# Optimization experiments

Hardware: AMD Instinct MI355X
Metric: run time of the kernel (lower is better)

The kernel has to match this reference:

```python
import jax, jax.numpy as jnp
import numpy as np

D = 64       # latent channels (d)
T = 512      # frame length, pinned by fc_1 = Linear(512*d//2, 512)
NUM_M = 64   # codebook size for source half (num_s = num_m)
NUM_N = 32   # codebook size for noise half (num_n = num_m // 2)
SCALE = 1.0  # soft-assignment temperature (self.scale)
K = 9        # BasicBlock conv kernel width


def conv1d(x, w, b):
    # x: (B, Cin, T), w: (Cout, Cin, K) -> (B, Cout, T), SAME padding
    y = jax.lax.conv_general_dilated(
        x, w, window_strides=(1,), padding='SAME',
        dimension_numbers=('NCH', 'OIH', 'NCH'))
    return y + b[None, :, None]


def basic_block(x, w1, b1, w2, b2, ws=None, bs=None):
    # Residual 1-D conv block: conv-relu-conv + shortcut, relu.
    h = jax.nn.relu(conv1d(x, w1, b1))
    h = conv1d(h, w2, b2)
    sc = x if ws is None else conv1d(x, ws, bs)
    return jax.nn.relu(h + sc)


def code_assign(x, means, scale):
    # VQ-style soft codebook assignment.
    # x: (B, C, T), means: (C, M)
    xt = jnp.swapaxes(x, 1, 2)  # (B, T, C)
    d2 = (jnp.sum(xt * xt, axis=-1, keepdims=True)
          - 2.0 * jnp.einsum('btc,cm->btm', xt, means)
          + jnp.sum(means * means, axis=0)[None, None, :])  # (B, T, M) squared dists
    prob = jax.nn.softmax(-scale * d2, axis=-1)              # soft assignment
    q = jnp.einsum('btm,cm->bct', prob, means)               # (B, C, T)
    arg_idx = jnp.argmin(d2, axis=-1)                        # (B, T) hard code index
    return q, arg_idx


def setup_inputs() -> dict:
    key = jax.random.key(0)
    ks = jax.random.split(key, 10)
    s = 0.05
    B = 1024
    return {
        'x': jax.random.normal(ks[0], (B, T), jnp.float32),
        'enc0_w1': jax.random.normal(ks[1], (D, 1, K), jnp.float32) * s,
        'enc0_b1': jnp.zeros((D,), jnp.float32),
        'enc0_w2': jax.random.normal(ks[2], (D, D, K), jnp.float32) * s,
        'enc0_b2': jnp.zeros((D,), jnp.float32),
        'enc0_ws': jax.random.normal(ks[3], (D, 1, 1), jnp.float32) * s,
        'enc0_bs': jnp.zeros((D,), jnp.float32),
        'enc_w': jax.random.normal(ks[4], (3, 2, D, D, K), jnp.float32) * s,
        'enc_b': jnp.zeros((3, 2, D), jnp.float32),
        'dec_w': jax.random.normal(ks[5], (3, 2, D // 2, D // 2, K), jnp.float32) * s,
        'dec_b': jnp.zeros((3, 2, D // 2), jnp.float32),
        'fc1_w': jax.random.normal(ks[6], (512, T * D // 2), jnp.float32) * 0.01,
        'fc1_b': jnp.zeros((512,), jnp.float32),
        'means_s': jax.random.uniform(ks[7], (D // 2, NUM_M), jnp.float32),
        'means_n': jax.random.uniform(ks[8], (D // 2, NUM_N), jnp.float32),
    }


def reference(x, enc0_w1, enc0_b1, enc0_w2, enc0_b2, enc0_ws, enc0_bs,
              enc_w, enc_b, dec_w, dec_b, fc1_w, fc1_b, means_s, means_n):
    # forward_half, stage == 1 (VQ coding active), soft=True
    B = x.shape[0]
    h = x[:, None, :]                                     # (B, 1, T)
    h = basic_block(h, enc0_w1, enc0_b1, enc0_w2, enc0_b2, enc0_ws, enc0_bs)
    h = jax.nn.relu(h)
    for i in range(3):
        h = basic_block(h, enc_w[i, 0], enc_b[i, 0], enc_w[i, 1], enc_b[i, 1])
    code_s = h[:, :D // 2, :]                             # (B, 32, T)
    code_n = h[:, D // 2:, :]
    q_s, idx_s = code_assign(code_s, means_s, SCALE)
    q_n, idx_n = code_assign(code_n, means_n, SCALE)

    def dec(z):
        for i in range(3):
            z = basic_block(z, dec_w[i, 0], dec_b[i, 0], dec_w[i, 1], dec_b[i, 1])
        flat = z.reshape(B, -1)                           # (B, T * D//2)
        return jnp.tanh(flat @ fc1_w.T + fc1_b)           # (B, 512)

    s_hat = dec(q_s)
    n_hat = dec(q_n)
    return s_hat, n_hat, idx_s, idx_n
```

## Files before the change

kernel.cpp:

```cpp
#include <hip/hip_runtime.h>
#include <math.h>


#define TB 512
#define BATCH 1024

__global__ __launch_bounds__(256) void transpose_w_f64_kernel(
    const float* __restrict__ w, double* __restrict__ wT, int C, int nmat) {
  int total = nmat * C * C * 9;
  for (int i = blockIdx.x * blockDim.x + threadIdx.x; i < total;
       i += gridDim.x * blockDim.x) {
    int mat = i / (C * C * 9);
    int r = i % (C * C * 9);
    int cout = r / (C * 9);
    int rem = r % (C * 9);
    int cin = rem / 9;
    int k = rem % 9;
    wT[mat * C * C * 9 + (k * C + cin) * C + cout] = (double)w[i];
  }
}

__global__ __launch_bounds__(256) void transpose_w_f32_kernel(
    const float* __restrict__ w, float* __restrict__ wT, int C, int nmat) {
  int total = nmat * C * C * 9;
  for (int i = blockIdx.x * blockDim.x + threadIdx.x; i < total;
       i += gridDim.x * blockDim.x) {
    int mat = i / (C * C * 9);
    int r = i % (C * C * 9);
    int cout = r / (C * 9);
    int rem = r % (C * 9);
    int cin = rem / 9;
    int k = rem % 9;
    wT[mat * C * C * 9 + (k * C + cin) * C + cout] = w[i];
  }
}

__global__ __launch_bounds__(256) void enc0_f64_kernel(
    const float* __restrict__ x, const float* __restrict__ w1,
    const float* __restrict__ b1, const double* __restrict__ w2T,
    const float* __restrict__ b2, const float* __restrict__ wsc,
    const float* __restrict__ bsc, double* __restrict__ out) {
  __shared__ double xs[80];
  __shared__ double w1s[576];
  __shared__ double b1s[64];
  __shared__ double mid[64 * 72];
  int b = blockIdx.y;
  int t0 = blockIdx.x * 64;
  int tid = threadIdx.x;
  if (tid < 80) {
    int t = t0 - 8 + tid;
    xs[tid] = (t >= 0 && t < TB) ? (double)x[b * TB + t] : 0.0;
  }
  for (int i = tid; i < 576; i += 256) w1s[i] = (double)w1[i];
  if (tid < 64) b1s[tid] = (double)b1[tid];
  __syncthreads();
  for (int e = tid; e < 64 * 72; e += 256) {
    int cout = e / 72, tt = e % 72;
    int t = t0 - 4 + tt;
    double acc = b1s[cout];
#pragma unroll
    for (int k = 0; k < 9; ++k) acc = fma(w1s[cout * 9 + k], xs[tt + k], acc);
    mid[e] = (t >= 0 && t < TB) ? fmax(acc, 0.0) : 0.0;
  }
  __syncthreads();
  int wave = __builtin_amdgcn_readfirstlane(tid >> 6);
  int lane = tid & 63;
  int cbase = wave * 16;
  double acc[16];
#pragma unroll
  for (int j = 0; j < 16; ++j) acc[j] = (double)b2[cbase + j];
  for (int cin = 0; cin < 64; ++cin) {
#pragma unroll
    for (int k = 0; k < 9; ++k) {
      double xv = mid[cin * 72 + lane + k];
      const double* wp = w2T + (k * 64 + cin) * 64 + cbase;
#pragma unroll
      for (int j = 0; j < 16; ++j) acc[j] = fma(xv, wp[j], acc[j]);
    }
  }
  double xc = xs[8 + lane];
#pragma unroll
  for (int j = 0; j < 16; ++j) {
    double v = acc[j] + fma((double)wsc[cbase + j], xc, (double)bsc[cbase + j]);
    out[(b * 64 + cbase + j) * TB + t0 + lane] = fmax(v, 0.0);
  }
}

template <bool SKIP>
__global__ __launch_bounds__(256) void conv64_f64_kernel(
    const double* __restrict__ in, const double* __restrict__ wT,
    const float* __restrict__ bias, const double* __restrict__ skip,
    double* __restrict__ out) {
  __shared__ double xs[64 * 72];
  int b = blockIdx.y;
  int t0 = blockIdx.x * 64;
  int tid = threadIdx.x;
  for (int i = tid; i < 64 * 72; i += 256) {
    int cin = i / 72, tt = i % 72;
    int t = t0 - 4 + tt;
    xs[i] = (t >= 0 && t < TB) ? in[(b * 64 + cin) * TB + t] : 0.0;
  }
  __syncthreads();
  int wave = __builtin_amdgcn_readfirstlane(tid >> 6);
  int lane = tid & 63;
  int cbase = wave * 16;
  double acc[16];
#pragma unroll
  for (int j = 0; j < 16; ++j) acc[j] = (double)bias[cbase + j];
  for (int cin = 0; cin < 64; ++cin) {
#pragma unroll
    for (int k = 0; k < 9; ++k) {
      double xv = xs[cin * 72 + lane + k];
      const double* wp = wT + (k * 64 + cin) * 64 + cbase;
#pragma unroll
      for (int j = 0; j < 16; ++j) acc[j] = fma(xv, wp[j], acc[j]);
    }
  }
  int t = t0 + lane;
#pragma unroll
  for (int j = 0; j < 16; ++j) {
    double v = acc[j];
    if constexpr (SKIP) v += skip[(b * 64 + cbase + j) * TB + t];
    out[(b * 64 + cbase + j) * TB + t] = fmax(v, 0.0);
  }
}

template <bool SKIP>
__global__ __launch_bounds__(256) void conv32_f32_kernel(
    const float* __restrict__ in, const float* __restrict__ wT,
    const float* __restrict__ bias, const float* __restrict__ skip,
    float* __restrict__ out) {
  constexpr int XW = 136;
  __shared__ float xs[32 * XW];
  int b = blockIdx.y;
  int t0 = blockIdx.x * 128;
  int tid = threadIdx.x;
  for (int i = tid; i < 32 * XW; i += 256) {
    int cin = i / XW, tt = i % XW;
    int t = t0 - 4 + tt;
    xs[i] = (t >= 0 && t < TB) ? in[(b * 32 + cin) * TB + t] : 0.f;
  }
  __syncthreads();
  int wave = __builtin_amdgcn_readfirstlane(tid >> 6);
  int lane = tid & 63;
  int cbase = (wave & 1) * 16;
  int ttl = (wave >> 1) * 64 + lane;
  float acc[16];
#pragma unroll
  for (int j = 0; j < 16; ++j) acc[j] = bias[cbase + j];
  for (int cin = 0; cin < 32; ++cin) {
#pragma unroll
    for (int k = 0; k < 9; ++k) {
      float xv = xs[cin * XW + ttl + k];
      const float* wp = wT + (k * 32 + cin) * 32 + cbase;
#pragma unroll
      for (int j = 0; j < 16; ++j) acc[j] = fmaf(xv, wp[j], acc[j]);
    }
  }
  int t = t0 + ttl;
#pragma unroll
  for (int j = 0; j < 16; ++j) {
    float v = acc[j];
    if constexpr (SKIP) v += skip[(b * 32 + cbase + j) * TB + t];
    out[(b * 32 + cbase + j) * TB + t] = fmaxf(v, 0.f);
  }
}

template <int M>
__global__ __launch_bounds__(256) void code_assign_kernel(
    const double* __restrict__ h, int coff, const float* __restrict__ means,
    float* __restrict__ q, float* __restrict__ idx_out) {
  __shared__ double ms[32 * M];
  __shared__ float msf[32 * M];
  __shared__ double msq[M];
  int b = blockIdx.y;
  int tid = threadIdx.x;
  int t = blockIdx.x * 256 + tid;
  for (int i = tid; i < 32 * M; i += 256) {
    float v = means[i];
    ms[i] = (double)v;
    msf[i] = v;
  }
  __syncthreads();
  if (tid < M) {
    double s = 0.0;
#pragma unroll
    for (int c = 0; c < 32; ++c) s = fma(ms[c * M + tid], ms[c * M + tid], s);
    msq[tid] = s;
  }
  __syncthreads();
  double xv[32];
  double sx = 0.0;
#pragma unroll
  for (int c = 0; c < 32; ++c) {
    xv[c] = h[(b * 64 + coff + c) * TB + t];
    sx = fma(xv[c], xv[c], sx);
  }
  double dmin = 1e300;
  int imin = 0;
  float ssum = 0.f;
  float qv[32];
#pragma unroll
  for (int c = 0; c < 32; ++c) qv[c] = 0.f;
  for (int m = 0; m < M; ++m) {
    double dot = 0.0;
#pragma unroll
    for (int c = 0; c < 32; ++c) dot = fma(xv[c], ms[c * M + m], dot);
    double d = sx - 2.0 * dot + msq[m];
    float p;
    if (d < dmin) {
      float f = expf((float)(d - dmin));
      ssum *= f;
#pragma unroll
      for (int c = 0; c < 32; ++c) qv[c] *= f;
      dmin = d;
      imin = m;
      p = 1.f;
    } else {
      p = expf((float)(dmin - d));
    }
    ssum += p;
#pragma unroll
    for (int c = 0; c < 32; ++c) qv[c] = fmaf(p, msf[c * M + m], qv[c]);
  }
  float inv = 1.f / ssum;
#pragma unroll
  for (int c = 0; c < 32; ++c) q[(b * 32 + c) * TB + t] = qv[c] * inv;
  idx_out[b * TB + t] = (float)imin;
}

__global__ __launch_bounds__(256) void fc_partial_gemm(
    const float* __restrict__ Z, const float* __restrict__ w,
    float* __restrict__ PB, int Mrows) {
  constexpr int BK = 32;
  constexpr int KC = 2048;
  __shared__ float As[BK][68];
  __shared__ float Bs[BK][68];
  int m0 = blockIdx.y * 64;
  int n0 = blockIdx.x * 64;
  int kbase = blockIdx.z * KC;
  int tid = threadIdx.x;
  int row = tid >> 2;
  int kq = (tid & 3) * 4;
  const float* zrow = Z + (size_t)(m0 + row) * 16384 + kbase;
  const float* wrow = w + (size_t)(n0 + row) * 16384 + kbase;
  int mg = tid >> 4;
  int ng = tid & 15;
  float acc[4][4] = {};
  for (int k0 = 0; k0 < KC; k0 += BK) {
    float4 a0 = *(const float4*)&zrow[k0 + kq];
    float4 a1 = *(const float4*)&zrow[k0 + kq + 16];
    float4 b0 = *(const float4*)&wrow[k0 + kq];
    float4 b1 = *(const float4*)&wrow[k0 + kq + 16];
    __syncthreads();
    As[kq + 0][row] = a0.x; As[kq + 1][row] = a0.y;
    As[kq + 2][row] = a0.z; As[kq + 3][row] = a0.w;
    As[kq + 16][row] = a1.x; As[kq + 17][row] = a1.y;
    As[kq + 18][row] = a1.z; As[kq + 19][row] = a1.w;
    Bs[kq + 0][row] = b0.x; Bs[kq + 1][row] = b0.y;
    Bs[kq + 2][row] = b0.z; Bs[kq + 3][row] = b0.w;
    Bs[kq + 16][row] = b1.x; Bs[kq + 17][row] = b1.y;
    Bs[kq + 18][row] = b1.z; Bs[kq + 19][row] = b1.w;
    __syncthreads();
#pragma unroll
    for (int kk = 0; kk < BK; ++kk) {
      float4 av = *(const float4*)&As[kk][mg * 4];
      float4 bv = *(const float4*)&Bs[kk][ng * 4];
      acc[0][0] = fmaf(av.x, bv.x, acc[0][0]);
      acc[0][1] = fmaf(av.x, bv.y, acc[0][1]);
      acc[0][2] = fmaf(av.x, bv.z, acc[0][2]);
      acc[0][3] = fmaf(av.x, bv.w, acc[0][3]);
      acc[1][0] = fmaf(av.y, bv.x, acc[1][0]);
      acc[1][1] = fmaf(av.y, bv.y, acc[1][1]);
      acc[1][2] = fmaf(av.y, bv.z, acc[1][2]);
      acc[1][3] = fmaf(av.y, bv.w, acc[1][3]);
      acc[2][0] = fmaf(av.z, bv.x, acc[2][0]);
      acc[2][1] = fmaf(av.z, bv.y, acc[2][1]);
      acc[2][2] = fmaf(av.z, bv.z, acc[2][2]);
      acc[2][3] = fmaf(av.z, bv.w, acc[2][3]);
      acc[3][0] = fmaf(av.w, bv.x, acc[3][0]);
      acc[3][1] = fmaf(av.w, bv.y, acc[3][1]);
      acc[3][2] = fmaf(av.w, bv.z, acc[3][2]);
      acc[3][3] = fmaf(av.w, bv.w, acc[3][3]);
    }
  }
  float* pbase = PB + (size_t)blockIdx.z * Mrows * 512;
#pragma unroll
  for (int mi = 0; mi < 4; ++mi) {
    float4 v = {acc[mi][0], acc[mi][1], acc[mi][2], acc[mi][3]};
    *(float4*)&pbase[(size_t)(m0 + mg * 4 + mi) * 512 + n0 + ng * 4] = v;
  }
}

__global__ __launch_bounds__(256) void fc_reduce_tanh(
    const float* __restrict__ PB, const float* __restrict__ bias,
    float* __restrict__ out, int Mrows, int rps, int c0) {
  constexpr int KS = 8;
  int idx = blockIdx.x * 256 + threadIdx.x;
  int m = idx >> 9, n = idx & 511;
  if (m >= Mrows) return;
  float s = bias[n];
#pragma unroll
  for (int ks = 0; ks < KS; ++ks)
    s += PB[((size_t)ks * Mrows + m) * 512 + n];
  int st = m / rps, rr = m - st * rps;
  out[((size_t)st * 1024 + c0 + rr) * 512 + n] = tanhf(s);
}

extern "C" void kernel_launch(void* const* d_in, const int* in_sizes, int n_in,
                              void* d_out, int out_size, void* d_ws,
                              size_t ws_size, hipStream_t stream) {
  const float* x = (const float*)d_in[0];
  const float* enc0_w1 = (const float*)d_in[1];
  const float* enc0_b1 = (const float*)d_in[2];
  const float* enc0_w2 = (const float*)d_in[3];
  const float* enc0_b2 = (const float*)d_in[4];
  const float* enc0_ws = (const float*)d_in[5];
  const float* enc0_bs = (const float*)d_in[6];
  const float* enc_w = (const float*)d_in[7];
  const float* enc_b = (const float*)d_in[8];
  const float* dec_w = (const float*)d_in[9];
  const float* dec_b = (const float*)d_in[10];
  const float* fc1_w = (const float*)d_in[11];
  const float* fc1_b = (const float*)d_in[12];
  const float* means_s = (const float*)d_in[13];
  const float* means_n = (const float*)d_in[14];

  const size_t WB = 2285568;
  int BC = 32;
  for (int c = 512; c >= 32; c >>= 1)
    if (WB + (size_t)c * 524288 <= ws_size) { BC = c; break; }

  double* wT0d = (double*)d_ws;
  double* wTed = wT0d + 36864;
  float* wTdf = (float*)(wTed + 221184);
  double* E0d = (double*)(wTdf + 55296);
  double* E1d = E0d + (size_t)BC * 32768;
  float* qs = (float*)E1d;
  float* qn = qs + (size_t)BC * 16384;
  float* D0 = qn + (size_t)BC * 16384;
  float* T1 = D0 + (size_t)BC * 16384;
  float* Dz = (float*)E0d;
  float* PB = Dz + (size_t)2 * BC * 16384;
  float* out = (float*)d_out;

  transpose_w_f64_kernel<<<dim3(144), 256, 0, stream>>>(enc0_w2, wT0d, 64, 1);
  transpose_w_f64_kernel<<<dim3(864), 256, 0, stream>>>(enc_w, wTed, 64, 6);
  transpose_w_f32_kernel<<<dim3(216), 256, 0, stream>>>(dec_w, wTdf, 32, 6);

  for (int c0 = 0; c0 < BATCH; c0 += BC) {
    const float* xb = x + (size_t)c0 * TB;

    enc0_f64_kernel<<<dim3(8, BC), 256, 0, stream>>>(
        xb, enc0_w1, enc0_b1, wT0d, enc0_b2, enc0_ws, enc0_bs, E0d);
    for (int i = 0; i < 3; ++i) {
      conv64_f64_kernel<false><<<dim3(8, BC), 256, 0, stream>>>(
          E0d, wTed + (2 * i) * 36864, enc_b + (2 * i) * 64, nullptr, E1d);
      conv64_f64_kernel<true><<<dim3(8, BC), 256, 0, stream>>>(
          E1d, wTed + (2 * i + 1) * 36864, enc_b + (2 * i + 1) * 64, E0d, E0d);
    }

    code_assign_kernel<64><<<dim3(2, BC), 256, 0, stream>>>(
        E0d, 0, means_s, qs, out + 2 * 524288 + (size_t)c0 * TB);
    code_assign_kernel<32><<<dim3(2, BC), 256, 0, stream>>>(
        E0d, 32, means_n, qn, out + 3 * 524288 + (size_t)c0 * TB);

    float* destS = Dz;
    float* destN = Dz + (size_t)BC * 16384;
    {
      float* outs[3] = {T1, qs, destS};
      const float* zin = qs;
      for (int i = 0; i < 3; ++i) {
        conv32_f32_kernel<false><<<dim3(4, BC), 256, 0, stream>>>(
            zin, wTdf + (2 * i) * 9216, dec_b + (2 * i) * 32, nullptr, D0);
        conv32_f32_kernel<true><<<dim3(4, BC), 256, 0, stream>>>(
            D0, wTdf + (2 * i + 1) * 9216, dec_b + (2 * i + 1) * 32, zin,
            outs[i]);
        zin = outs[i];
      }
    }
    {
      float* outs[3] = {T1, qn, destN};
      const float* zin = qn;
      for (int i = 0; i < 3; ++i) {
        conv32_f32_kernel<false><<<dim3(4, BC), 256, 0, stream>>>(
            zin, wTdf + (2 * i) * 9216, dec_b + (2 * i) * 32, nullptr, D0);
        conv32_f32_kernel<true><<<dim3(4, BC), 256, 0, stream>>>(
            D0, wTdf + (2 * i + 1) * 9216, dec_b + (2 * i + 1) * 32, zin,
            outs[i]);
        zin = outs[i];
      }
    }

    fc_partial_gemm<<<dim3(8, (2 * BC) / 64, 8), 256, 0, stream>>>(
        Dz, fc1_w, PB, 2 * BC);
    fc_reduce_tanh<<<dim3((2 * BC * 512) / 256), 256, 0, stream>>>(
        PB, fc1_b, out, 2 * BC, BC, c0);
  }
}
```

Baseline: 8.481 ms.

## Remap fp64 conv64 threads to output channels with register sliding window over time

The 64-channel fp64 conv kernels now assign each lane one output channel and each wave a 16-step time slab. Each lane keeps a 24-element input window in registers and does one coalesced weight load per tap, instead of reading 16 wave-uniform weights per tap and an input value from shared memory per tap. Results go through a padded shared-memory transpose so global stores stay coalesced. This cuts LDS traffic and scalar weight loads per FMA, at the cost of extra registers, more vector-memory weight loads and an added transpose with two more barriers.

```diff
diff --git a/kernel.cpp b/kernel.cpp
--- a/kernel.cpp
+++ b/kernel.cpp
@@ -35,12 +35,31 @@
   }
 }
 
+__device__ __forceinline__ void conv64_body(const double* __restrict__ xs,
+                                            const double* __restrict__ wT,
+                                            double acc[16], int lane,
+                                            int wslab) {
+  for (int cin = 0; cin < 64; ++cin) {
+    const double* xr = xs + cin * 72 + wslab * 16;
+    double xwin[24];
+#pragma unroll
+    for (int i = 0; i < 24; ++i) xwin[i] = xr[i];
+    const double* wp = wT + cin * 64 + lane;
+#pragma unroll
+    for (int k = 0; k < 9; ++k) {
+      double w = wp[k * 4096];
+#pragma unroll
+      for (int t = 0; t < 16; ++t) acc[t] = fma(w, xwin[t + k], acc[t]);
+    }
+  }
+}
+
 __global__ __launch_bounds__(256) void enc0_f64_kernel(
     const float* __restrict__ x, const float* __restrict__ w1,
     const float* __restrict__ b1, const double* __restrict__ w2T,
     const float* __restrict__ b2, const float* __restrict__ wsc,
     const float* __restrict__ bsc, double* __restrict__ out) {
-  __shared__ double xs[80];
+  __shared__ double xs0[80];
   __shared__ double w1s[576];
   __shared__ double b1s[64];
   __shared__ double mid[64 * 72];
@@ -49,7 +68,7 @@
   int tid = threadIdx.x;
   if (tid < 80) {
     int t = t0 - 8 + tid;
-    xs[tid] = (t >= 0 && t < TB) ? (double)x[b * TB + t] : 0.0;
+    xs0[tid] = (t >= 0 && t < TB) ? (double)x[b * TB + t] : 0.0;
   }
   for (int i = tid; i < 576; i += 256) w1s[i] = (double)w1[i];
   if (tid < 64) b1s[tid] = (double)b1[tid];
@@ -59,30 +78,27 @@
     int t = t0 - 4 + tt;
     double acc = b1s[cout];
 #pragma unroll
-    for (int k = 0; k < 9; ++k) acc = fma(w1s[cout * 9 + k], xs[tt + k], acc);
+    for (int k = 0; k < 9; ++k) acc = fma(w1s[cout * 9 + k], xs0[tt + k], acc);
     mid[e] = (t >= 0 && t < TB) ? fmax(acc, 0.0) : 0.0;
   }
   __syncthreads();
-  int wave = __builtin_amdgcn_readfirstlane(tid >> 6);
+  int wave = tid >> 6;
   int lane = tid & 63;
-  int cbase = wave * 16;
   double acc[16];
-#pragma unroll
-  for (int j = 0; j < 16; ++j) acc[j] = (double)b2[cbase + j];
-  for (int cin = 0; cin < 64; ++cin) {
-#pragma unroll
-    for (int k = 0; k < 9; ++k) {
-      double xv = mid[cin * 72 + lane + k];
-      const double* wp = w2T + (k * 64 + cin) * 64 + cbase;
-#pragma unroll
-      for (int j = 0; j < 16; ++j) acc[j] = fma(xv, wp[j], acc[j]);
-    }
-  }
-  double xc = xs[8 + lane];
-#pragma unroll
-  for (int j = 0; j < 16; ++j) {
-    double v = acc[j] + fma((double)wsc[cbase + j], xc, (double)bsc[cbase + j]);
-    out[(b * 64 + cbase + j) * TB + t0 + lane] = fmax(v, 0.0);
+  double bz = (double)b2[lane];
+#pragma unroll
+  for (int t = 0; t < 16; ++t) acc[t] = bz;
+  conv64_body(mid, w2T, acc, lane, wave);
+  __syncthreads();
+  double* T = mid;
+#pragma unroll
+  for (int t = 0; t < 16; ++t) T[lane * 65 + wave * 16 + t] = acc[t];
+  __syncthreads();
+  for (int i = tid; i < 4096; i += 256) {
+    int cout = i >> 6, tt = i & 63;
+    double v = T[cout * 65 + tt] +
+               fma((double)wsc[cout], xs0[8 + tt], (double)bsc[cout]);
+    out[(b * 64 + cout) * TB + t0 + tt] = fmax(v, 0.0);
   }
 }
 
@@ -101,27 +117,23 @@
     xs[i] = (t >= 0 && t < TB) ? in[(b * 64 + cin) * TB + t] : 0.0;
   }
   __syncthreads();
-  int wave = __builtin_amdgcn_readfirstlane(tid >> 6);
+  int wave = tid >> 6;
   int lane = tid & 63;
-  int cbase = wave * 16;
   double acc[16];
-#pragma unroll
-  for (int j = 0; j < 16; ++j) acc[j] = (double)bias[cbase + j];
-  for (int cin = 0; cin < 64; ++cin) {
-#pragma unroll
-    for (int k = 0; k < 9; ++k) {
-      double xv = xs[cin * 72 + lane + k];
-      const double* wp = wT + (k * 64 + cin) * 64 + cbase;
-#pragma unroll
-      for (int j = 0; j < 16; ++j) acc[j] = fma(xv, wp[j], acc[j]);
-    }
-  }
-  int t = t0 + lane;
-#pragma unroll
-  for (int j = 0; j < 16; ++j) {
-    double v = acc[j];
-    if constexpr (SKIP) v += skip[(b * 64 + cbase + j) * TB + t];
-    out[(b * 64 + cbase + j) * TB + t] = fmax(v, 0.0);
+  double bz = (double)bias[lane];
+#pragma unroll
+  for (int t = 0; t < 16; ++t) acc[t] = bz;
+  conv64_body(xs, wT, acc, lane, wave);
+  __syncthreads();
+  double* T = xs;
+#pragma unroll
+  for (int t = 0; t < 16; ++t) T[lane * 65 + wave * 16 + t] = acc[t];
+  __syncthreads();
+  for (int i = tid; i < 4096; i += 256) {
+    int cout = i >> 6, tt = i & 63;
+    double v = T[cout * 65 + tt];
+    if constexpr (SKIP) v += skip[(b * 64 + cout) * TB + t0 + tt];
+    out[(b * 64 + cout) * TB + t0 + tt] = fmax(v, 0.0);
   }
 }
 
```

New measurement: 8.487 ms. No clear change (+0.1%).
